# Kernel optimization log

Hardware: AMD Instinct MI355X
Metric: run time of the kernel (lower is better)

## Reference

```python
import jax, jax.numpy as jnp
import numpy as np

B = 262144
I = 128   # input_len
H = 128   # h_len (must equal c_len structurally)
C = 128   # c_len
O = 128   # output_len
STD = 0.05  # keras random_normal default stddev


def setup_inputs() -> dict:
    key = jax.random.key(0)
    ks = jax.random.split(key, 14)
    inp = {
        "c_": jax.random.normal(ks[0], (B, C), dtype=jnp.float32),
        "h_": jax.random.normal(ks[1], (B, H), dtype=jnp.float32),
        "x": jax.random.normal(ks[2], (B, I), dtype=jnp.float32),
        # gate weights [C, I+H] and biases [C]
        "w": jax.random.normal(ks[3], (C, I + H), dtype=jnp.float32) * STD,
        "wi": jax.random.normal(ks[4], (C, I + H), dtype=jnp.float32) * STD,
        "wf": jax.random.normal(ks[5], (C, I + H), dtype=jnp.float32) * STD,
        "wo": jax.random.normal(ks[6], (C, I + H), dtype=jnp.float32) * STD,
        "w_out": jax.random.normal(ks[7], (O, H), dtype=jnp.float32) * STD,
        "b": jax.random.normal(ks[8], (C,), dtype=jnp.float32) * STD,
        "bi": jax.random.normal(ks[9], (C,), dtype=jnp.float32) * STD,
        "bf": jax.random.normal(ks[10], (C,), dtype=jnp.float32) * STD,
        "bo": jax.random.normal(ks[11], (C,), dtype=jnp.float32) * STD,
        "b_out": jax.random.normal(ks[12], (O,), dtype=jnp.float32) * STD,
    }
    return inp


def reference(c_, h_, x, w, wi, wf, wo, w_out, b, bi, bf, bo, b_out):
    # [B, I+H]
    xh = jnp.concatenate([x, h_], axis=-1)
    # Fuse the 4 gate matmuls into one GEMM with stacked weights [4C, I+H]
    W = jnp.concatenate([w, wi, wf, wo], axis=0)
    Bv = jnp.concatenate([b, bi, bf, bo], axis=0)
    gates = xh @ W.T + Bv                      # [B, 4C]
    gz, gi, gf, go = jnp.split(gates, 4, axis=-1)
    z = jnp.tanh(gz)
    zi = jax.nn.sigmoid(gi)
    zf = jax.nn.sigmoid(gf)
    zo = jax.nn.sigmoid(go)
    c = zf * c_ + zi * z                       # [B, C]
    h = zo * jnp.tanh(c)                       # [B, C] (== H)
    y = jax.nn.sigmoid(h @ w_out.T + b_out)    # [B, O]
    return (c, h, y)
```

## Files before the change

kernel.cpp:

```cpp
#include <hip/hip_runtime.h>

#define TB 262144

typedef short bf16x8 __attribute__((ext_vector_type(8)));
typedef float f32x4 __attribute__((ext_vector_type(4)));

__device__ __forceinline__ unsigned short f2bf(float f) {
  unsigned int u = __float_as_uint(f);
  unsigned int r = (u + 0x7fffu + ((u >> 16) & 1u)) >> 16;
  return (unsigned short)r;
}
__device__ __forceinline__ float sigmoid_f(float x) {
  return __builtin_amdgcn_rcpf(1.f + __expf(-x));
}
__device__ __forceinline__ float tanh_f(float x) {
  return 1.f - 2.f * __builtin_amdgcn_rcpf(__expf(2.f * x) + 1.f);
}

__global__ void wconv_kernel(const float* __restrict__ w, const float* __restrict__ wi,
                             const float* __restrict__ wf, const float* __restrict__ wo,
                             const float* __restrict__ wout, unsigned short* __restrict__ dst) {
  int i = blockIdx.x * 256 + threadIdx.x;
  float v;
  if (i < 32768) v = w[i];
  else if (i < 65536) v = wi[i - 32768];
  else if (i < 98304) v = wf[i - 65536];
  else if (i < 131072) v = wo[i - 98304];
  else v = wout[i - 131072];
  dst[i] = f2bf(v);
}

__global__ __launch_bounds__(256, 3) void lstm_main(
    const float* __restrict__ c_prev, const float* __restrict__ h_prev,
    const float* __restrict__ x, const unsigned short* __restrict__ wbf,
    const float* __restrict__ b, const float* __restrict__ bi,
    const float* __restrict__ bf_, const float* __restrict__ bo,
    const float* __restrict__ b_out,
    float* __restrict__ out_c, float* __restrict__ out_h, float* __restrict__ out_y) {
  __shared__ unsigned short us_xh[16384];
  __shared__ unsigned short us_h[8192];

  const int tid = threadIdx.x;
  const int wave = tid >> 6;
  const int lane = tid & 63;
  const int lr = lane & 15;
  const int lq = lane >> 4;
  const int row0 = blockIdx.x * 64;
  const int j0 = wave * 32;

  {
    const int tr = tid >> 5;
    const int tc = (tid & 31) * 4;
#pragma unroll
    for (int it = 0; it < 8; ++it) {
      const int r = it * 8 + tr;
      const float4 vx = *reinterpret_cast<const float4*>(&x[(size_t)(row0 + r) * 128 + tc]);
      const float4 vh = *reinterpret_cast<const float4*>(&h_prev[(size_t)(row0 + r) * 128 + tc]);
      ushort4 ux; ux.x = f2bf(vx.x); ux.y = f2bf(vx.y); ux.z = f2bf(vx.z); ux.w = f2bf(vx.w);
      ushort4 uh; uh.x = f2bf(vh.x); uh.y = f2bf(vh.y); uh.z = f2bf(vh.z); uh.w = f2bf(vh.w);
      const int sw = (r & 7) << 3;
      *reinterpret_cast<ushort4*>(&us_xh[(r * 256 + tc) ^ sw]) = ux;
      *reinterpret_cast<ushort4*>(&us_xh[(r * 256 + 128 + tc) ^ sw]) = uh;
    }
  }
  __syncthreads();

  float cv0[4][4];
  float hv0[4][4];

#pragma unroll
  for (int jc = 0; jc < 2; ++jc) {
    const int jcol = j0 + jc * 16 + lr;

    float cpre[4][4];
#pragma unroll
    for (int rf = 0; rf < 4; ++rf) {
#pragma unroll
      for (int i = 0; i < 4; ++i) {
        cpre[rf][i] = c_prev[(size_t)(row0 + rf * 16 + lq * 4 + i) * 128 + jcol];
      }
    }
    const float bz_s = b[jcol];
    const float bi_s = bi[jcol];
    const float bf_s = bf_[jcol];
    const float bo_s = bo[jcol];

    f32x4 acc[4][4];
    const f32x4 zero = {0.f, 0.f, 0.f, 0.f};
#pragma unroll
    for (int rf = 0; rf < 4; ++rf) {
#pragma unroll
      for (int g = 0; g < 4; ++g) acc[rf][g] = zero;
    }

#pragma unroll 2
    for (int kk = 0; kk < 8; ++kk) {
      const int kb = kk * 32 + lq * 8;
      const int woff = jcol * 256 + kb;
      const bf16x8 bz8 = *reinterpret_cast<const bf16x8*>(&wbf[woff]);
      const bf16x8 bi8 = *reinterpret_cast<const bf16x8*>(&wbf[32768 + woff]);
      const bf16x8 bf8 = *reinterpret_cast<const bf16x8*>(&wbf[65536 + woff]);
      const bf16x8 bo8 = *reinterpret_cast<const bf16x8*>(&wbf[98304 + woff]);
#pragma unroll
      for (int rf = 0; rf < 4; ++rf) {
        const int r = rf * 16 + lr;
        const bf16x8 a8 =
            *reinterpret_cast<const bf16x8*>(&us_xh[(r * 256 + kb) ^ ((r & 7) << 3)]);
        acc[rf][0] = __builtin_amdgcn_mfma_f32_16x16x32_bf16(a8, bz8, acc[rf][0], 0, 0, 0);
        acc[rf][1] = __builtin_amdgcn_mfma_f32_16x16x32_bf16(a8, bi8, acc[rf][1], 0, 0, 0);
        acc[rf][2] = __builtin_amdgcn_mfma_f32_16x16x32_bf16(a8, bf8, acc[rf][2], 0, 0, 0);
        acc[rf][3] = __builtin_amdgcn_mfma_f32_16x16x32_bf16(a8, bo8, acc[rf][3], 0, 0, 0);
      }
    }

#pragma unroll
    for (int rf = 0; rf < 4; ++rf) {
#pragma unroll
      for (int i = 0; i < 4; ++i) {
        const int r = rf * 16 + lq * 4 + i;
        const float z  = tanh_f(acc[rf][0][i] + bz_s);
        const float zi = sigmoid_f(acc[rf][1][i] + bi_s);
        const float zf = sigmoid_f(acc[rf][2][i] + bf_s);
        const float zo = sigmoid_f(acc[rf][3][i] + bo_s);
        const float cvv = zf * cpre[rf][i] + zi * z;
        const float hvv = zo * tanh_f(cvv);
        us_h[(r * 128 + jcol) ^ ((r & 7) << 3)] = f2bf(hvv);
        if (jc == 0) {
          cv0[rf][i] = cvv;
          hv0[rf][i] = hvv;
        } else {
          const size_t gi = (size_t)(row0 + r) * 128 + j0 + lr;
          out_c[gi]      = cv0[rf][i];
          out_c[gi + 16] = cvv;
          out_h[gi]      = hv0[rf][i];
          out_h[gi + 16] = hvv;
        }
      }
    }
  }
  __syncthreads();

  const int rb2 = wave * 16;
  bf16x8 a2[4];
#pragma unroll
  for (int ks = 0; ks < 4; ++ks) {
    const int r = rb2 + lr;
    const int k = ks * 32 + lq * 8;
    a2[ks] = *reinterpret_cast<const bf16x8*>(&us_h[(r * 128 + k) ^ ((r & 7) << 3)]);
  }
#pragma unroll
  for (int t = 0; t < 4; ++t) {
    const int n0 = t * 32 + lr;
    const int n1 = n0 + 16;
    const f32x4 zero = {0.f, 0.f, 0.f, 0.f};
    f32x4 acc2a = zero, acc2b = zero;
#pragma unroll
    for (int ks = 0; ks < 4; ++ks) {
      const bf16x8 bw0 =
          *reinterpret_cast<const bf16x8*>(&wbf[131072 + n0 * 128 + ks * 32 + lq * 8]);
      const bf16x8 bw1 =
          *reinterpret_cast<const bf16x8*>(&wbf[131072 + n1 * 128 + ks * 32 + lq * 8]);
      acc2a = __builtin_amdgcn_mfma_f32_16x16x32_bf16(a2[ks], bw0, acc2a, 0, 0, 0);
      acc2b = __builtin_amdgcn_mfma_f32_16x16x32_bf16(a2[ks], bw1, acc2b, 0, 0, 0);
    }
    const float bya = b_out[n0];
    const float byb = b_out[n1];
#pragma unroll
    for (int i = 0; i < 4; ++i) {
      const size_t gr = (size_t)(row0 + rb2 + lq * 4 + i) * 128;
      out_y[gr + n0] = sigmoid_f(acc2a[i] + bya);
      out_y[gr + n1] = sigmoid_f(acc2b[i] + byb);
    }
  }
}

extern "C" void kernel_launch(void* const* d_in, const int* in_sizes, int n_in,
                              void* d_out, int out_size, void* d_ws, size_t ws_size,
                              hipStream_t stream) {
  const float* c_    = (const float*)d_in[0];
  const float* h_    = (const float*)d_in[1];
  const float* x     = (const float*)d_in[2];
  const float* w     = (const float*)d_in[3];
  const float* wi    = (const float*)d_in[4];
  const float* wf    = (const float*)d_in[5];
  const float* wo    = (const float*)d_in[6];
  const float* wout  = (const float*)d_in[7];
  const float* b     = (const float*)d_in[8];
  const float* bi    = (const float*)d_in[9];
  const float* bf_   = (const float*)d_in[10];
  const float* bo    = (const float*)d_in[11];
  const float* b_out = (const float*)d_in[12];

  unsigned short* wbf = (unsigned short*)d_ws;
  float* out_c = (float*)d_out;
  float* out_h = out_c + (size_t)TB * 128;
  float* out_y = out_h + (size_t)TB * 128;

  hipLaunchKernelGGL(wconv_kernel, dim3(576), dim3(256), 0, stream,
                     w, wi, wf, wo, wout, wbf);
  hipLaunchKernelGGL(lstm_main, dim3(4096), dim3(256), 0, stream,
                     c_, h_, x, wbf, b, bi, bf_, bo, b_out, out_c, out_h, out_y);
}
```

Before: 317.8 us.

## Switch to 32x32x16 MFMA with 32-row blocks and doubled grid

Replaces the 16x16x32 MFMA tiling with 32x32x16 MFMA tiles and halves the rows per block from 64 to 32, doubling the grid to 8192 blocks. Each wave now computes its 32-column gate slice for all 32 rows in a single pass, and the output GEMM runs one 32x32 tile per wave. LDS use is halved, and c/h/y outputs are written directly from the accumulator layout. The aim is fewer instructions and more resident blocks. The cost is that weight fragments are reloaded from global memory for half as many rows per load, which doubles weight traffic per output row.

```diff
diff --git a/kernel.cpp b/kernel.cpp
--- a/kernel.cpp
+++ b/kernel.cpp
@@ -3,7 +3,7 @@
 #define TB 262144
 
 typedef short bf16x8 __attribute__((ext_vector_type(8)));
-typedef float f32x4 __attribute__((ext_vector_type(4)));
+typedef float f32x16 __attribute__((ext_vector_type(16)));
 
 __device__ __forceinline__ unsigned short f2bf(float f) {
   unsigned int u = __float_as_uint(f);
@@ -37,140 +37,100 @@
     const float* __restrict__ bf_, const float* __restrict__ bo,
     const float* __restrict__ b_out,
     float* __restrict__ out_c, float* __restrict__ out_h, float* __restrict__ out_y) {
-  __shared__ unsigned short us_xh[16384];
-  __shared__ unsigned short us_h[8192];
+  __shared__ unsigned short us_xh[8192];
+  __shared__ unsigned short us_h[4096];
 
   const int tid = threadIdx.x;
   const int wave = tid >> 6;
   const int lane = tid & 63;
-  const int lr = lane & 15;
-  const int lq = lane >> 4;
-  const int row0 = blockIdx.x * 64;
+  const int l31 = lane & 31;
+  const int lhi = lane >> 5;
+  const int kb_lane = lhi * 8;
+  const int row0 = blockIdx.x * 32;
   const int j0 = wave * 32;
+  const int jcol = j0 + l31;
 
   {
-    const int tr = tid >> 5;
-    const int tc = (tid & 31) * 4;
 #pragma unroll
-    for (int it = 0; it < 8; ++it) {
-      const int r = it * 8 + tr;
-      const float4 vx = *reinterpret_cast<const float4*>(&x[(size_t)(row0 + r) * 128 + tc]);
-      const float4 vh = *reinterpret_cast<const float4*>(&h_prev[(size_t)(row0 + r) * 128 + tc]);
+    for (int it = 0; it < 4; ++it) {
+      const int cid = it * 256 + tid;
+      const int r = cid >> 5;
+      const int c4 = (cid & 31) * 4;
+      const float4 vx = *reinterpret_cast<const float4*>(&x[(size_t)(row0 + r) * 128 + c4]);
       ushort4 ux; ux.x = f2bf(vx.x); ux.y = f2bf(vx.y); ux.z = f2bf(vx.z); ux.w = f2bf(vx.w);
+      *reinterpret_cast<ushort4*>(&us_xh[(r * 256 + c4) ^ ((r & 7) << 3)]) = ux;
+    }
+#pragma unroll
+    for (int it = 0; it < 4; ++it) {
+      const int cid = it * 256 + tid;
+      const int r = cid >> 5;
+      const int c4 = (cid & 31) * 4;
+      const float4 vh = *reinterpret_cast<const float4*>(&h_prev[(size_t)(row0 + r) * 128 + c4]);
       ushort4 uh; uh.x = f2bf(vh.x); uh.y = f2bf(vh.y); uh.z = f2bf(vh.z); uh.w = f2bf(vh.w);
-      const int sw = (r & 7) << 3;
-      *reinterpret_cast<ushort4*>(&us_xh[(r * 256 + tc) ^ sw]) = ux;
-      *reinterpret_cast<ushort4*>(&us_xh[(r * 256 + 128 + tc) ^ sw]) = uh;
+      *reinterpret_cast<ushort4*>(&us_xh[(r * 256 + 128 + c4) ^ ((r & 7) << 3)]) = uh;
     }
   }
   __syncthreads();
 
-  float cv0[4][4];
-  float hv0[4][4];
+  float cpre[16];
+#pragma unroll
+  for (int reg = 0; reg < 16; ++reg) {
+    const int r = (reg & 3) + 8 * (reg >> 2) + 4 * lhi;
+    cpre[reg] = c_prev[(size_t)(row0 + r) * 128 + jcol];
+  }
 
+  f32x16 accz = {}, acci = {}, accf = {}, acco = {};
 #pragma unroll
-  for (int jc = 0; jc < 2; ++jc) {
-    const int jcol = j0 + jc * 16 + lr;
+  for (int kk = 0; kk < 16; ++kk) {
+    const int kb = kk * 16 + kb_lane;
+    const bf16x8 a8 =
+        *reinterpret_cast<const bf16x8*>(&us_xh[(l31 * 256 + kb) ^ ((l31 & 7) << 3)]);
+    const int woff = jcol * 256 + kb;
+    const bf16x8 bz8 = *reinterpret_cast<const bf16x8*>(&wbf[woff]);
+    const bf16x8 bi8 = *reinterpret_cast<const bf16x8*>(&wbf[32768 + woff]);
+    const bf16x8 bf8 = *reinterpret_cast<const bf16x8*>(&wbf[65536 + woff]);
+    const bf16x8 bo8 = *reinterpret_cast<const bf16x8*>(&wbf[98304 + woff]);
+    accz = __builtin_amdgcn_mfma_f32_32x32x16_bf16(a8, bz8, accz, 0, 0, 0);
+    acci = __builtin_amdgcn_mfma_f32_32x32x16_bf16(a8, bi8, acci, 0, 0, 0);
+    accf = __builtin_amdgcn_mfma_f32_32x32x16_bf16(a8, bf8, accf, 0, 0, 0);
+    acco = __builtin_amdgcn_mfma_f32_32x32x16_bf16(a8, bo8, acco, 0, 0, 0);
+  }
 
-    float cpre[4][4];
+  const float bz_s = b[jcol];
+  const float bi_s = bi[jcol];
+  const float bf_s = bf_[jcol];
+  const float bo_s = bo[jcol];
 #pragma unroll
-    for (int rf = 0; rf < 4; ++rf) {
-#pragma unroll
-      for (int i = 0; i < 4; ++i) {
-        cpre[rf][i] = c_prev[(size_t)(row0 + rf * 16 + lq * 4 + i) * 128 + jcol];
-      }
-    }
-    const float bz_s = b[jcol];
-    const float bi_s = bi[jcol];
-    const float bf_s = bf_[jcol];
-    const float bo_s = bo[jcol];
-
-    f32x4 acc[4][4];
-    const f32x4 zero = {0.f, 0.f, 0.f, 0.f};
-#pragma unroll
-    for (int rf = 0; rf < 4; ++rf) {
-#pragma unroll
-      for (int g = 0; g < 4; ++g) acc[rf][g] = zero;
-    }
-
-#pragma unroll 2
-    for (int kk = 0; kk < 8; ++kk) {
-      const int kb = kk * 32 + lq * 8;
-      const int woff = jcol * 256 + kb;
-      const bf16x8 bz8 = *reinterpret_cast<const bf16x8*>(&wbf[woff]);
-      const bf16x8 bi8 = *reinterpret_cast<const bf16x8*>(&wbf[32768 + woff]);
-      const bf16x8 bf8 = *reinterpret_cast<const bf16x8*>(&wbf[65536 + woff]);
-      const bf16x8 bo8 = *reinterpret_cast<const bf16x8*>(&wbf[98304 + woff]);
-#pragma unroll
-      for (int rf = 0; rf < 4; ++rf) {
-        const int r = rf * 16 + lr;
-        const bf16x8 a8 =
-            *reinterpret_cast<const bf16x8*>(&us_xh[(r * 256 + kb) ^ ((r & 7) << 3)]);
-        acc[rf][0] = __builtin_amdgcn_mfma_f32_16x16x32_bf16(a8, bz8, acc[rf][0], 0, 0, 0);
-        acc[rf][1] = __builtin_amdgcn_mfma_f32_16x16x32_bf16(a8, bi8, acc[rf][1], 0, 0, 0);
-        acc[rf][2] = __builtin_amdgcn_mfma_f32_16x16x32_bf16(a8, bf8, acc[rf][2], 0, 0, 0);
-        acc[rf][3] = __builtin_amdgcn_mfma_f32_16x16x32_bf16(a8, bo8, acc[rf][3], 0, 0, 0);
-      }
-    }
-
-#pragma unroll
-    for (int rf = 0; rf < 4; ++rf) {
-#pragma unroll
-      for (int i = 0; i < 4; ++i) {
-        const int r = rf * 16 + lq * 4 + i;
-        const float z  = tanh_f(acc[rf][0][i] + bz_s);
-        const float zi = sigmoid_f(acc[rf][1][i] + bi_s);
-        const float zf = sigmoid_f(acc[rf][2][i] + bf_s);
-        const float zo = sigmoid_f(acc[rf][3][i] + bo_s);
-        const float cvv = zf * cpre[rf][i] + zi * z;
-        const float hvv = zo * tanh_f(cvv);
-        us_h[(r * 128 + jcol) ^ ((r & 7) << 3)] = f2bf(hvv);
-        if (jc == 0) {
-          cv0[rf][i] = cvv;
-          hv0[rf][i] = hvv;
-        } else {
-          const size_t gi = (size_t)(row0 + r) * 128 + j0 + lr;
-          out_c[gi]      = cv0[rf][i];
-          out_c[gi + 16] = cvv;
-          out_h[gi]      = hv0[rf][i];
-          out_h[gi + 16] = hvv;
-        }
-      }
-    }
+  for (int reg = 0; reg < 16; ++reg) {
+    const int r = (reg & 3) + 8 * (reg >> 2) + 4 * lhi;
+    const size_t gi = (size_t)(row0 + r) * 128 + jcol;
+    const float z  = tanh_f(accz[reg] + bz_s);
+    const float zi = sigmoid_f(acci[reg] + bi_s);
+    const float zf = sigmoid_f(accf[reg] + bf_s);
+    const float zo = sigmoid_f(acco[reg] + bo_s);
+    const float cvv = zf * cpre[reg] + zi * z;
+    const float hvv = zo * tanh_f(cvv);
+    out_c[gi] = cvv;
+    out_h[gi] = hvv;
+    us_h[(r * 128 + jcol) ^ ((r & 7) << 3)] = f2bf(hvv);
   }
   __syncthreads();
 
-  const int rb2 = wave * 16;
-  bf16x8 a2[4];
+  f32x16 accy = {};
 #pragma unroll
-  for (int ks = 0; ks < 4; ++ks) {
-    const int r = rb2 + lr;
-    const int k = ks * 32 + lq * 8;
-    a2[ks] = *reinterpret_cast<const bf16x8*>(&us_h[(r * 128 + k) ^ ((r & 7) << 3)]);
+  for (int ks = 0; ks < 8; ++ks) {
+    const int kb = ks * 16 + kb_lane;
+    const bf16x8 a8 =
+        *reinterpret_cast<const bf16x8*>(&us_h[(l31 * 128 + kb) ^ ((l31 & 7) << 3)]);
+    const bf16x8 bw =
+        *reinterpret_cast<const bf16x8*>(&wbf[131072 + jcol * 128 + kb]);
+    accy = __builtin_amdgcn_mfma_f32_32x32x16_bf16(a8, bw, accy, 0, 0, 0);
   }
+  const float by_s = b_out[jcol];
 #pragma unroll
-  for (int t = 0; t < 4; ++t) {
-    const int n0 = t * 32 + lr;
-    const int n1 = n0 + 16;
-    const f32x4 zero = {0.f, 0.f, 0.f, 0.f};
-    f32x4 acc2a = zero, acc2b = zero;
-#pragma unroll
-    for (int ks = 0; ks < 4; ++ks) {
-      const bf16x8 bw0 =
-          *reinterpret_cast<const bf16x8*>(&wbf[131072 + n0 * 128 + ks * 32 + lq * 8]);
-      const bf16x8 bw1 =
-          *reinterpret_cast<const bf16x8*>(&wbf[131072 + n1 * 128 + ks * 32 + lq * 8]);
-      acc2a = __builtin_amdgcn_mfma_f32_16x16x32_bf16(a2[ks], bw0, acc2a, 0, 0, 0);
-      acc2b = __builtin_amdgcn_mfma_f32_16x16x32_bf16(a2[ks], bw1, acc2b, 0, 0, 0);
-    }
-    const float bya = b_out[n0];
-    const float byb = b_out[n1];
-#pragma unroll
-    for (int i = 0; i < 4; ++i) {
-      const size_t gr = (size_t)(row0 + rb2 + lq * 4 + i) * 128;
-      out_y[gr + n0] = sigmoid_f(acc2a[i] + bya);
-      out_y[gr + n1] = sigmoid_f(acc2b[i] + byb);
-    }
+  for (int reg = 0; reg < 16; ++reg) {
+    const int r = (reg & 3) + 8 * (reg >> 2) + 4 * lhi;
+    out_y[(size_t)(row0 + r) * 128 + jcol] = sigmoid_f(accy[reg] + by_s);
   }
 }
 
@@ -198,6 +158,6 @@
 
   hipLaunchKernelGGL(wconv_kernel, dim3(576), dim3(256), 0, stream,
                      w, wi, wf, wo, wout, wbf);
-  hipLaunchKernelGGL(lstm_main, dim3(4096), dim3(256), 0, stream,
+  hipLaunchKernelGGL(lstm_main, dim3(8192), dim3(256), 0, stream,
                      c_, h_, x, wbf, b, bi, bf_, bo, b_out, out_c, out_h, out_y);
 }
```

Result: slower. 390.9 us (+23.0%).
